# Kernel optimization log

Hardware: AMD Instinct MI355X
Metric: run time of the kernel (lower is better)

Reference implementation:

```python
import jax, jax.numpy as jnp
import numpy as np

B, C, H, W = 32, 512, 32, 32
HEADS = 8
HD = C // HEADS  # 64
BN_EPS = 1e-5


def setup_inputs() -> dict:
    key = jax.random.key(0)
    ks = jax.random.split(key, 8)
    s = 0.02  # trunc_normal std for Linear weights
    x = jax.random.normal(ks[0], (B, C, H, W), jnp.float32)
    Wq = jax.random.normal(ks[1], (C, C), jnp.float32) * s
    Wk = jax.random.normal(ks[2], (C, C), jnp.float32) * s
    Wv = jax.random.normal(ks[3], (C, C), jnp.float32) * s
    # depthwise 3x3 kernel, kaiming fan_out (fan_out = 3*3*1 per group)
    dw_w = jax.random.normal(ks[4], (C, 1, 3, 3), jnp.float32) * np.sqrt(2.0 / 9.0)
    bn_gamma = jnp.ones((C,), jnp.float32)
    bn_beta = jnp.zeros((C,), jnp.float32)
    temperature = jnp.ones((HEADS, 1, 1), jnp.float32)
    Wp = jax.random.normal(ks[5], (C, C), jnp.float32) * s
    bp = jnp.zeros((C,), jnp.float32)
    return {"x": x, "Wq": Wq, "Wk": Wk, "Wv": Wv, "dw_w": dw_w,
            "bn_gamma": bn_gamma, "bn_beta": bn_beta,
            "temperature": temperature, "Wp": Wp, "bp": bp}


def _l2norm(t):
    # torch F.normalize: x / max(||x||, eps)
    n = jnp.sqrt(jnp.sum(t * t, axis=-1, keepdims=True))
    return t / jnp.maximum(n, 1e-12)


def _forward(x, Wq, Wk, Wv, dw_w, bn_gamma, bn_beta, temperature, Wp, bp):
    b, c, h, w = x.shape
    n = h * w
    x_flat = x.transpose(0, 2, 3, 1).reshape(b, n, c)  # [B,N,C]

    q = (x_flat @ Wq.T).reshape(b, n, HEADS, HD).transpose(0, 2, 3, 1)  # [B,h,d,N]
    k = (x_flat @ Wk.T).reshape(b, n, HEADS, HD).transpose(0, 2, 3, 1)
    q = _l2norm(q)
    k = _l2norm(k)

    attn = jnp.einsum('bhdn,bhen->bhde', q, k) * temperature  # [B,h,d,d]
    attn = jax.nn.softmax(attn, axis=-1)

    v_content = x_flat @ Wv.T  # [B,N,C]

    # gated value path: DWConv -> BatchNorm (batch stats, train mode) -> SiLU
    g = jax.lax.conv_general_dilated(
        x, dw_w, window_strides=(1, 1), padding=((1, 1), (1, 1)),
        feature_group_count=c, dimension_numbers=('NCHW', 'OIHW', 'NCHW'))
    mu = jnp.mean(g, axis=(0, 2, 3), keepdims=True)
    var = jnp.var(g, axis=(0, 2, 3), keepdims=True)
    g = (g - mu) * jax.lax.rsqrt(var + BN_EPS)
    g = g * bn_gamma[None, :, None, None] + bn_beta[None, :, None, None]
    g = g * jax.nn.sigmoid(g)  # SiLU
    v_gate = g.transpose(0, 2, 3, 1).reshape(b, n, c)

    v = (v_content * v_gate).reshape(b, n, HEADS, HD).transpose(0, 2, 3, 1)  # [B,h,d,N]
    out = jnp.einsum('bhde,bhen->bhdn', attn, v)  # [B,h,d,N]
    out = out.transpose(0, 3, 1, 2).reshape(b, n, c)  # [B,N,C]
    out = out @ Wp.T + bp
    return out.reshape(b, h, w, c).transpose(0, 3, 1, 2)  # [B,C,H,W]


def reference(x, Wq, Wk, Wv, dw_w, bn_gamma, bn_beta, temperature, Wp, bp):
    return _forward(x, Wq, Wk, Wv, dw_w, bn_gamma, bn_beta, temperature, Wp, bp)
```

## Files before the change

kernel.cpp:

```cpp
#include <hip/hip_runtime.h>
#include <stdint.h>

#define BATCH 32
#define CCH   512
#define NPIX  1024
#define HEADS 8
#define QKV_M 1536

typedef short bf16x8 __attribute__((ext_vector_type(8)));
typedef float f32x4 __attribute__((ext_vector_type(4)));

__device__ inline float bf2f(unsigned short u) {
  union { float f; uint32_t i; } t; t.i = ((uint32_t)u) << 16; return t.f;
}
__device__ inline unsigned short f2bf(float f) {
  union { float f; uint32_t u; } t; t.f = f;
  uint32_t u = t.u;
  return (unsigned short)((u + 0x7FFFu + ((u >> 16) & 1u)) >> 16);
}

__device__ inline void gl_lds16(const unsigned short* g, unsigned short* l) {
  __builtin_amdgcn_global_load_lds(
      (const __attribute__((address_space(1))) uint32_t*)g,
      (__attribute__((address_space(3))) uint32_t*)l, 16, 0, 0);
}

__global__ void convert_w(const float* __restrict__ Wq, const float* __restrict__ Wk,
                          const float* __restrict__ Wv, const float* __restrict__ Wp,
                          unsigned short* __restrict__ wcat,
                          unsigned short* __restrict__ wpb) {
  int i = (blockIdx.x * 256 + threadIdx.x) * 4;
  union { ushort4 u4; unsigned short s[4]; } o;
  f32x4 a;
  a = *(const f32x4*)&Wq[i];
  for (int j = 0; j < 4; j++) o.s[j] = f2bf(a[j]);
  *(ushort4*)&wcat[i] = o.u4;
  a = *(const f32x4*)&Wk[i];
  for (int j = 0; j < 4; j++) o.s[j] = f2bf(a[j]);
  *(ushort4*)&wcat[CCH * CCH + i] = o.u4;
  a = *(const f32x4*)&Wv[i];
  for (int j = 0; j < 4; j++) o.s[j] = f2bf(a[j]);
  *(ushort4*)&wcat[2 * CCH * CCH + i] = o.u4;
  a = *(const f32x4*)&Wp[i];
  for (int j = 0; j < 4; j++) o.s[j] = f2bf(a[j]);
  *(ushort4*)&wpb[i] = o.u4;
}

__global__ void transpose_f2b(const float* __restrict__ in,
                              unsigned short* __restrict__ out, int R, int Cc) {
  __shared__ float tile[32][33];
  int b = blockIdx.z;
  int c0 = blockIdx.x * 32;
  int r0 = blockIdx.y * 32;
  const float* inb = in + (size_t)b * R * Cc;
  unsigned short* outb = out + (size_t)b * R * Cc;
  int tx = threadIdx.x, ty = threadIdx.y;
  for (int i = 0; i < 4; i++) {
    int r = ty + i * 8;
    tile[r][tx] = inb[(size_t)(r0 + r) * Cc + c0 + tx];
  }
  __syncthreads();
  for (int i = 0; i < 4; i++) {
    int r = ty + i * 8;
    outb[(size_t)(c0 + r) * R + r0 + tx] = f2bf(tile[tx][r]);
  }
}

template <bool OUT_F32>
__launch_bounds__(256)
__global__ void gemm_bt(const unsigned short* __restrict__ A,
                        const unsigned short* __restrict__ X,
                        void* __restrict__ Cout,
                        const float* __restrict__ bias,
                        int M, int N, int K) {
  __shared__ __align__(16) unsigned short As[128 * 32];
  __shared__ __align__(16) unsigned short Bs[128 * 32];
  int b  = blockIdx.z;
  int m0 = blockIdx.y * 128;
  int n0 = blockIdx.x * 128;
  const unsigned short* Xb = X + (size_t)b * N * K;
  int tid = threadIdx.x;
  int lane = tid & 63;
  int wave = tid >> 6;
  int wm = wave >> 1, wn = wave & 1;
  int quad = lane >> 4, l16 = lane & 15;

  f32x4 acc[4][4];
  f32x4 zero = {0.f, 0.f, 0.f, 0.f};
  for (int i = 0; i < 4; i++)
    for (int j = 0; j < 4; j++) acc[i][j] = zero;

  int srow = wave * 32 + (lane >> 2);
  int skp  = (lane & 3) * 8;
  const unsigned short* Ag = A  + (size_t)(m0 + srow) * K + skp;
  const unsigned short* Xg = Xb + (size_t)(n0 + srow) * K + skp;
  unsigned short* Al = &As[wave * 1024];
  unsigned short* Bl = &Bs[wave * 1024];

  for (int k0 = 0; k0 < K; k0 += 32) {
    gl_lds16(Ag + k0,            Al);
    gl_lds16(Ag + 16 * K + k0,   Al + 512);
    gl_lds16(Xg + k0,            Bl);
    gl_lds16(Xg + 16 * K + k0,   Bl + 512);
    __syncthreads();
    bf16x8 af[4], bfr[4];
    for (int i = 0; i < 4; i++)
      af[i] = *(const bf16x8*)&As[(wm * 64 + i * 16 + l16) * 32 + quad * 8];
    for (int j = 0; j < 4; j++)
      bfr[j] = *(const bf16x8*)&Bs[(wn * 64 + j * 16 + l16) * 32 + quad * 8];
    for (int i = 0; i < 4; i++)
      for (int j = 0; j < 4; j++)
        acc[i][j] = __builtin_amdgcn_mfma_f32_16x16x32_bf16(af[i], bfr[j], acc[i][j], 0, 0, 0);
    __syncthreads();
  }

  for (int i = 0; i < 4; i++) {
    int gmb = m0 + wm * 64 + i * 16 + quad * 4;
    for (int j = 0; j < 4; j++) {
      int gn = n0 + wn * 64 + j * 16 + l16;
      for (int r = 0; r < 4; r++) {
        int gm = gmb + r;
        float v = acc[i][j][r];
        if (OUT_F32) {
          v += bias[gm];
          ((float*)Cout)[(size_t)b * M * N + (size_t)gm * N + gn] = v;
        } else {
          ((unsigned short*)Cout)[(size_t)b * M * N + (size_t)gm * N + gn] = f2bf(v);
        }
      }
    }
  }
}

__global__ void l2norm_qk(unsigned short* __restrict__ qkv, int nb) {
  int id = blockIdx.x * 4 + (threadIdx.x >> 6);
  int lane = threadIdx.x & 63;
  int total = nb * CCH;
  int isK = id >= total;
  int r = isK ? id - total : id;
  int b = r >> 9, c = r & 511;
  unsigned short* p = qkv + ((size_t)b * QKV_M + (isK ? CCH : 0) + c) * NPIX;
  union { uint4 q4[2]; unsigned short s[16]; } u;
  u.q4[0] = *(const uint4*)&p[lane * 16];
  u.q4[1] = *(const uint4*)&p[lane * 16 + 8];
  float s = 0.f;
  for (int i = 0; i < 16; i++) { float f = bf2f(u.s[i]); s += f * f; }
  for (int off = 32; off > 0; off >>= 1) s += __shfl_down(s, off);
  s = __shfl(s, 0);
  float scale = 1.f / fmaxf(sqrtf(s), 1e-12f);
  for (int i = 0; i < 16; i++) u.s[i] = f2bf(bf2f(u.s[i]) * scale);
  *(uint4*)&p[lane * 16] = u.q4[0];
  *(uint4*)&p[lane * 16 + 8] = u.q4[1];
}

__global__ void dw_stats(const float* __restrict__ x,
                         const float* __restrict__ wgt,
                         float* __restrict__ s1, float* __restrict__ s2) {
  int c = blockIdx.x, b = blockIdx.y;
  __shared__ __align__(16) float plane[NPIX];
  const float* xp = x + ((size_t)b * CCH + c) * NPIX;
  *(f32x4*)&plane[threadIdx.x * 4] = *(const f32x4*)&xp[threadIdx.x * 4];
  __syncthreads();
  float w[9];
  for (int i = 0; i < 9; i++) w[i] = wgt[c * 9 + i];
  float a1 = 0.f, a2 = 0.f;
  for (int pi = 0; pi < 4; pi++) {
    int p = threadIdx.x + pi * 256;
    int h = p >> 5, wc = p & 31;
    float v = 0.f;
    for (int dh = -1; dh <= 1; dh++)
      for (int dw = -1; dw <= 1; dw++) {
        int hh = h + dh, ww = wc + dw;
        if (hh >= 0 && hh < 32 && ww >= 0 && ww < 32)
          v += w[(dh + 1) * 3 + dw + 1] * plane[hh * 32 + ww];
      }
    a1 += v; a2 += v * v;
  }
  for (int off = 32; off > 0; off >>= 1) {
    a1 += __shfl_down(a1, off);
    a2 += __shfl_down(a2, off);
  }
  __shared__ float r1[4], r2[4];
  int wv = threadIdx.x >> 6;
  if ((threadIdx.x & 63) == 0) { r1[wv] = a1; r2[wv] = a2; }
  __syncthreads();
  if (threadIdx.x == 0) {
    atomicAdd(&s1[c], r1[0] + r1[1] + r1[2] + r1[3]);
    atomicAdd(&s2[c], r2[0] + r2[1] + r2[2] + r2[3]);
  }
}

__global__ void gate_apply(const float* __restrict__ x,
                           const float* __restrict__ wgt,
                           const float* __restrict__ s1, const float* __restrict__ s2,
                           const float* __restrict__ gamma,
                           const float* __restrict__ beta,
                           unsigned short* __restrict__ qkv) {
  int c = blockIdx.x, b = blockIdx.y;
  __shared__ __align__(16) float plane[NPIX];
  const float* xp = x + ((size_t)b * CCH + c) * NPIX;
  unsigned short* vp = qkv + ((size_t)b * QKV_M + 2 * CCH + c) * NPIX;
  *(f32x4*)&plane[threadIdx.x * 4] = *(const f32x4*)&xp[threadIdx.x * 4];
  __syncthreads();
  float w[9];
  for (int i = 0; i < 9; i++) w[i] = wgt[c * 9 + i];
  const float invn = 1.f / 32768.f;
  float mean = s1[c] * invn;
  float var = fmaxf(s2[c] * invn - mean * mean, 0.f);
  float rstd = rsqrtf(var + 1e-5f);
  float ga = gamma[c], be = beta[c];
  for (int pi = 0; pi < 4; pi++) {
    int p = threadIdx.x + pi * 256;
    int h = p >> 5, wc = p & 31;
    float val = 0.f;
    for (int dh = -1; dh <= 1; dh++)
      for (int dw = -1; dw <= 1; dw++) {
        int hh = h + dh, ww = wc + dw;
        if (hh >= 0 && hh < 32 && ww >= 0 && ww < 32)
          val += w[(dh + 1) * 3 + dw + 1] * plane[hh * 32 + ww];
      }
    float g = (val - mean) * rstd * ga + be;
    float sg = g / (1.f + __expf(-g));
    vp[p] = f2bf(bf2f(vp[p]) * sg);
  }
}

__launch_bounds__(256)
__global__ void attn_k(const unsigned short* __restrict__ qkv,
                       const float* __restrict__ temp,
                       unsigned short* __restrict__ aoT) {
  int bh = blockIdx.x;
  int b = bh >> 3, h = bh & 7;
  const unsigned short* Q = qkv + ((size_t)b * QKV_M + h * 64) * NPIX;
  const unsigned short* K = Q + (size_t)CCH * NPIX;
  const unsigned short* V = Q + (size_t)2 * CCH * NPIX;
  unsigned short* Ob = aoT + (size_t)b * NPIX * CCH + h * 64;
  int tid = threadIdx.x, lane = tid & 63, wave = tid >> 6;
  int quad = lane >> 4, l16 = lane & 15;

  __shared__ __align__(16) float Sf[64][65];
  __shared__ __align__(16) unsigned short Ps[64][72];
  __shared__ __align__(16) unsigned short Vt[4][16][72];
  __shared__ float redm[4][64], reds[4][64];

  f32x4 zero = {0.f, 0.f, 0.f, 0.f};
  f32x4 acc[4];
  for (int j = 0; j < 4; j++) acc[j] = zero;
  for (int n0 = 0; n0 < NPIX; n0 += 32) {
    bf16x8 a = *(const bf16x8*)&Q[(size_t)(wave * 16 + l16) * NPIX + n0 + quad * 8];
    for (int j = 0; j < 4; j++) {
      bf16x8 bb = *(const bf16x8*)&K[(size_t)(j * 16 + l16) * NPIX + n0 + quad * 8];
      acc[j] = __builtin_amdgcn_mfma_f32_16x16x32_bf16(a, bb, acc[j], 0, 0, 0);
    }
  }
  float tmp = temp[h];
  for (int j = 0; j < 4; j++)
    for (int r = 0; r < 4; r++)
      Sf[wave * 16 + quad * 4 + r][j * 16 + l16] = acc[j][r] * tmp;
  __syncthreads();

  {
    int row = tid & 63, seg = tid >> 6;
    float pm = -1e30f;
    for (int i = 0; i < 16; i++) pm = fmaxf(pm, Sf[row][seg * 16 + i]);
    redm[seg][row] = pm;
    __syncthreads();
    float m = fmaxf(fmaxf(redm[0][row], redm[1][row]),
                    fmaxf(redm[2][row], redm[3][row]));
    float ps = 0.f;
    for (int i = 0; i < 16; i++) ps += __expf(Sf[row][seg * 16 + i] - m);
    reds[seg][row] = ps;
    __syncthreads();
    float inv = 1.f / (reds[0][row] + reds[1][row] + reds[2][row] + reds[3][row]);
    for (int i = 0; i < 16; i++)
      Ps[row][seg * 16 + i] = f2bf(__expf(Sf[row][seg * 16 + i] - m) * inv);
  }
  __syncthreads();

  bf16x8 Pf[4][2];
  for (int j = 0; j < 4; j++)
    for (int ks = 0; ks < 2; ks++)
      Pf[j][ks] = *(const bf16x8*)&Ps[j * 16 + l16][ks * 32 + quad * 8];

  int e1 = lane >> 1, noff = (lane & 1) * 8;
  for (int nt = 0; nt < 16; nt++) {
    int n0 = wave * 256 + nt * 16;
    union { uint4 q; unsigned short s[8]; } g0, g1;
    g0.q = *(const uint4*)&V[(size_t)e1 * NPIX + n0 + noff];
    g1.q = *(const uint4*)&V[(size_t)(e1 + 32) * NPIX + n0 + noff];
    for (int jj = 0; jj < 8; jj++) {
      Vt[wave][noff + jj][e1]      = g0.s[jj];
      Vt[wave][noff + jj][e1 + 32] = g1.s[jj];
    }
    __builtin_amdgcn_sched_barrier(0);
    bf16x8 Af0 = *(const bf16x8*)&Vt[wave][l16][quad * 8];
    bf16x8 Af1 = *(const bf16x8*)&Vt[wave][l16][32 + quad * 8];
    f32x4 oacc[4];
    for (int j = 0; j < 4; j++) {
      oacc[j] = __builtin_amdgcn_mfma_f32_16x16x32_bf16(Af0, Pf[j][0], zero, 0, 0, 0);
      oacc[j] = __builtin_amdgcn_mfma_f32_16x16x32_bf16(Af1, Pf[j][1], oacc[j], 0, 0, 0);
    }
    __builtin_amdgcn_sched_barrier(0);
    for (int j = 0; j < 4; j++)
      for (int r = 0; r < 4; r++)
        Ob[(size_t)(n0 + quad * 4 + r) * CCH + j * 16 + l16] = f2bf(oacc[j][r]);
  }
}

extern "C" void kernel_launch(void* const* d_in, const int* in_sizes, int n_in,
                              void* d_out, int out_size, void* d_ws, size_t ws_size,
                              hipStream_t stream) {
  const float* x     = (const float*)d_in[0];
  const float* Wq    = (const float*)d_in[1];
  const float* Wk    = (const float*)d_in[2];
  const float* Wv    = (const float*)d_in[3];
  const float* dww   = (const float*)d_in[4];
  const float* gamma = (const float*)d_in[5];
  const float* beta  = (const float*)d_in[6];
  const float* temp  = (const float*)d_in[7];
  const float* Wp    = (const float*)d_in[8];
  const float* bp    = (const float*)d_in[9];
  float* out = (float*)d_out;

  char* ws = (char*)d_ws;
  unsigned short* wcat = (unsigned short*)ws;
  unsigned short* wpb  = wcat + (size_t)QKV_M * CCH;
  float* s1 = (float*)(wpb + (size_t)CCH * CCH);
  float* s2 = s1 + CCH;
  char* dyn = (char*)(s2 + CCH);
  size_t fixed = (size_t)(dyn - ws);
  size_t per_b = ((size_t)NPIX * CCH + (size_t)QKV_M * NPIX) * 2;
  int BC = BATCH;
  while (BC > 1 && fixed + (size_t)BC * per_b > ws_size) BC >>= 1;
  unsigned short* xT  = (unsigned short*)dyn;
  unsigned short* qkv = xT + (size_t)BC * NPIX * CCH;

  convert_w<<<CCH * CCH / 1024, 256, 0, stream>>>(Wq, Wk, Wv, Wp, wcat, wpb);
  hipMemsetAsync(s1, 0, 2 * CCH * sizeof(float), stream);
  dw_stats<<<dim3(CCH, BATCH), 256, 0, stream>>>(x, dww, s1, s2);

  for (int b0 = 0; b0 < BATCH; b0 += BC) {
    const float* xc = x + (size_t)b0 * CCH * NPIX;
    float* outc = out + (size_t)b0 * CCH * NPIX;
    transpose_f2b<<<dim3(NPIX / 32, CCH / 32, BC), dim3(32, 8), 0, stream>>>(
        xc, xT, CCH, NPIX);
    gemm_bt<false><<<dim3(NPIX / 128, QKV_M / 128, BC), 256, 0, stream>>>(
        wcat, xT, qkv, nullptr, QKV_M, NPIX, CCH);
    l2norm_qk<<<BC * 256, 256, 0, stream>>>(qkv, BC);
    gate_apply<<<dim3(CCH, BC), 256, 0, stream>>>(xc, dww, s1, s2, gamma, beta, qkv);
    attn_k<<<BC * HEADS, 256, 0, stream>>>(qkv, temp, xT);
    gemm_bt<true><<<dim3(NPIX / 128, CCH / 128, BC), 256, 0, stream>>>(
        wpb, xT, outc, bp, CCH, NPIX, CCH);
  }
}
```

Before: 350.9 us.

## Fold L2 norm into attention scores, split attention, widen GEMM K-tile with swizzle

Drops the separate l2norm pass over Q and K. Row norms are now taken from the diagonal MFMA products inside the score kernel and applied as scales to the 64x64 score matrix. Attention is split into a score/softmax kernel writing P to workspace and a P·V kernel launched with four times as many blocks, which prefetches V and stages output through LDS for coalesced 16-byte stores. The GEMM now loads a 64-wide K tile with an XOR-swizzled LDS layout, halving barrier count and reducing bank conflicts. The norms come from bf16 unnormalized values rather than normalized-then-rounded ones, so numerics shift slightly, and P adds a small workspace round trip.

```diff
diff --git a/kernel.cpp b/kernel.cpp
--- a/kernel.cpp
+++ b/kernel.cpp
@@ -73,8 +73,8 @@
                         void* __restrict__ Cout,
                         const float* __restrict__ bias,
                         int M, int N, int K) {
-  __shared__ __align__(16) unsigned short As[128 * 32];
-  __shared__ __align__(16) unsigned short Bs[128 * 32];
+  __shared__ __align__(16) unsigned short As[128 * 64];
+  __shared__ __align__(16) unsigned short Bs[128 * 64];
   int b  = blockIdx.z;
   int m0 = blockIdx.y * 128;
   int n0 = blockIdx.x * 128;
@@ -90,27 +90,31 @@
   for (int i = 0; i < 4; i++)
     for (int j = 0; j < 4; j++) acc[i][j] = zero;
 
-  int srow = wave * 32 + (lane >> 2);
-  int skp  = (lane & 3) * 8;
-  const unsigned short* Ag = A  + (size_t)(m0 + srow) * K + skp;
-  const unsigned short* Xg = Xb + (size_t)(n0 + srow) * K + skp;
-  unsigned short* Al = &As[wave * 1024];
-  unsigned short* Bl = &Bs[wave * 1024];
-
-  for (int k0 = 0; k0 < K; k0 += 32) {
-    gl_lds16(Ag + k0,            Al);
-    gl_lds16(Ag + 16 * K + k0,   Al + 512);
-    gl_lds16(Xg + k0,            Bl);
-    gl_lds16(Xg + 16 * K + k0,   Bl + 512);
+  int r8 = lane >> 3;
+  int sw = ((lane & 7) ^ r8) * 8;
+  const unsigned short* Ag = A  + (size_t)(m0 + wave * 32 + r8) * K + sw;
+  const unsigned short* Xg = Xb + (size_t)(n0 + wave * 32 + r8) * K + sw;
+  unsigned short* Al = &As[wave * 32 * 64];
+  unsigned short* Bl = &Bs[wave * 32 * 64];
+
+  for (int k0 = 0; k0 < K; k0 += 64) {
+    for (int i = 0; i < 4; i++) {
+      gl_lds16(Ag + k0 + i * 8 * K, Al + i * 8 * 64);
+      gl_lds16(Xg + k0 + i * 8 * K, Bl + i * 8 * 64);
+    }
     __syncthreads();
-    bf16x8 af[4], bfr[4];
-    for (int i = 0; i < 4; i++)
-      af[i] = *(const bf16x8*)&As[(wm * 64 + i * 16 + l16) * 32 + quad * 8];
-    for (int j = 0; j < 4; j++)
-      bfr[j] = *(const bf16x8*)&Bs[(wn * 64 + j * 16 + l16) * 32 + quad * 8];
-    for (int i = 0; i < 4; i++)
-      for (int j = 0; j < 4; j++)
-        acc[i][j] = __builtin_amdgcn_mfma_f32_16x16x32_bf16(af[i], bfr[j], acc[i][j], 0, 0, 0);
+    bf16x8 af[2][4], bfr[2][4];
+    for (int ks = 0; ks < 2; ks++)
+      for (int i = 0; i < 4; i++) {
+        int ch = ((ks * 4 + quad) ^ (l16 & 7)) * 8;
+        af[ks][i]  = *(const bf16x8*)&As[(wm * 64 + i * 16 + l16) * 64 + ch];
+        bfr[ks][i] = *(const bf16x8*)&Bs[(wn * 64 + i * 16 + l16) * 64 + ch];
+      }
+    for (int ks = 0; ks < 2; ks++)
+      for (int i = 0; i < 4; i++)
+        for (int j = 0; j < 4; j++)
+          acc[i][j] = __builtin_amdgcn_mfma_f32_16x16x32_bf16(
+              af[ks][i], bfr[ks][j], acc[i][j], 0, 0, 0);
     __syncthreads();
   }
 
@@ -130,27 +134,6 @@
       }
     }
   }
-}
-
-__global__ void l2norm_qk(unsigned short* __restrict__ qkv, int nb) {
-  int id = blockIdx.x * 4 + (threadIdx.x >> 6);
-  int lane = threadIdx.x & 63;
-  int total = nb * CCH;
-  int isK = id >= total;
-  int r = isK ? id - total : id;
-  int b = r >> 9, c = r & 511;
-  unsigned short* p = qkv + ((size_t)b * QKV_M + (isK ? CCH : 0) + c) * NPIX;
-  union { uint4 q4[2]; unsigned short s[16]; } u;
-  u.q4[0] = *(const uint4*)&p[lane * 16];
-  u.q4[1] = *(const uint4*)&p[lane * 16 + 8];
-  float s = 0.f;
-  for (int i = 0; i < 16; i++) { float f = bf2f(u.s[i]); s += f * f; }
-  for (int off = 32; off > 0; off >>= 1) s += __shfl_down(s, off);
-  s = __shfl(s, 0);
-  float scale = 1.f / fmaxf(sqrtf(s), 1e-12f);
-  for (int i = 0; i < 16; i++) u.s[i] = f2bf(bf2f(u.s[i]) * scale);
-  *(uint4*)&p[lane * 16] = u.q4[0];
-  *(uint4*)&p[lane * 16 + 8] = u.q4[1];
 }
 
 __global__ void dw_stats(const float* __restrict__ x,
@@ -226,73 +209,110 @@
 }
 
 __launch_bounds__(256)
-__global__ void attn_k(const unsigned short* __restrict__ qkv,
+__global__ void attn_s(const unsigned short* __restrict__ qkv,
                        const float* __restrict__ temp,
-                       unsigned short* __restrict__ aoT) {
+                       unsigned short* __restrict__ P) {
   int bh = blockIdx.x;
   int b = bh >> 3, h = bh & 7;
   const unsigned short* Q = qkv + ((size_t)b * QKV_M + h * 64) * NPIX;
   const unsigned short* K = Q + (size_t)CCH * NPIX;
-  const unsigned short* V = Q + (size_t)2 * CCH * NPIX;
+  int tid = threadIdx.x, lane = tid & 63, wave = tid >> 6;
+  int quad = lane >> 4, l16 = lane & 15;
+
+  __shared__ __align__(16) float Sf[64][65];
+  __shared__ float qq[64], kk[64], invq[64], invk[64];
+  __shared__ float redm[4][64], reds[4][64];
+
+  f32x4 zero = {0.f, 0.f, 0.f, 0.f};
+  f32x4 acc[4], accQ = zero, accK = zero;
+  for (int j = 0; j < 4; j++) acc[j] = zero;
+  for (int n0 = 0; n0 < NPIX; n0 += 32) {
+    bf16x8 a  = *(const bf16x8*)&Q[(size_t)(wave * 16 + l16) * NPIX + n0 + quad * 8];
+    bf16x8 ak = *(const bf16x8*)&K[(size_t)(wave * 16 + l16) * NPIX + n0 + quad * 8];
+    accQ = __builtin_amdgcn_mfma_f32_16x16x32_bf16(a, a, accQ, 0, 0, 0);
+    accK = __builtin_amdgcn_mfma_f32_16x16x32_bf16(ak, ak, accK, 0, 0, 0);
+    for (int j = 0; j < 4; j++) {
+      bf16x8 bb = *(const bf16x8*)&K[(size_t)(j * 16 + l16) * NPIX + n0 + quad * 8];
+      acc[j] = __builtin_amdgcn_mfma_f32_16x16x32_bf16(a, bb, acc[j], 0, 0, 0);
+    }
+  }
+  for (int j = 0; j < 4; j++)
+    for (int r = 0; r < 4; r++)
+      Sf[wave * 16 + quad * 4 + r][j * 16 + l16] = acc[j][r];
+  for (int r = 0; r < 4; r++)
+    if (l16 == quad * 4 + r) {
+      qq[wave * 16 + l16] = accQ[r];
+      kk[wave * 16 + l16] = accK[r];
+    }
+  __syncthreads();
+  if (tid < 64) invq[tid] = 1.f / fmaxf(sqrtf(qq[tid]), 1e-12f);
+  else if (tid < 128) invk[tid - 64] = 1.f / fmaxf(sqrtf(kk[tid - 64]), 1e-12f);
+  __syncthreads();
+
+  int row = tid & 63, seg = tid >> 6;
+  float fq = temp[h] * invq[row];
+  float v[16], pm = -1e30f;
+  for (int i = 0; i < 16; i++) {
+    v[i] = Sf[row][seg * 16 + i] * fq * invk[seg * 16 + i];
+    pm = fmaxf(pm, v[i]);
+  }
+  redm[seg][row] = pm;
+  __syncthreads();
+  float m = fmaxf(fmaxf(redm[0][row], redm[1][row]),
+                  fmaxf(redm[2][row], redm[3][row]));
+  float ps = 0.f;
+  for (int i = 0; i < 16; i++) { v[i] = __expf(v[i] - m); ps += v[i]; }
+  reds[seg][row] = ps;
+  __syncthreads();
+  float inv = 1.f / (reds[0][row] + reds[1][row] + reds[2][row] + reds[3][row]);
+  union { uint4 q4[2]; unsigned short s[16]; } u;
+  for (int i = 0; i < 16; i++) u.s[i] = f2bf(v[i] * inv);
+  unsigned short* Pp = P + ((size_t)bh * 64 + row) * 64 + seg * 16;
+  *(uint4*)&Pp[0] = u.q4[0];
+  *(uint4*)&Pp[8] = u.q4[1];
+}
+
+__launch_bounds__(256)
+__global__ void attn_o(const unsigned short* __restrict__ qkv,
+                       const unsigned short* __restrict__ P,
+                       unsigned short* __restrict__ aoT) {
+  int blk = blockIdx.x;
+  int nc = blk & 3, bh = blk >> 2;
+  int b = bh >> 3, h = bh & 7;
+  const unsigned short* V = qkv + ((size_t)b * QKV_M + 2 * CCH + h * 64) * NPIX;
   unsigned short* Ob = aoT + (size_t)b * NPIX * CCH + h * 64;
   int tid = threadIdx.x, lane = tid & 63, wave = tid >> 6;
   int quad = lane >> 4, l16 = lane & 15;
 
-  __shared__ __align__(16) float Sf[64][65];
-  __shared__ __align__(16) unsigned short Ps[64][72];
   __shared__ __align__(16) unsigned short Vt[4][16][72];
-  __shared__ float redm[4][64], reds[4][64];
-
-  f32x4 zero = {0.f, 0.f, 0.f, 0.f};
-  f32x4 acc[4];
-  for (int j = 0; j < 4; j++) acc[j] = zero;
-  for (int n0 = 0; n0 < NPIX; n0 += 32) {
-    bf16x8 a = *(const bf16x8*)&Q[(size_t)(wave * 16 + l16) * NPIX + n0 + quad * 8];
-    for (int j = 0; j < 4; j++) {
-      bf16x8 bb = *(const bf16x8*)&K[(size_t)(j * 16 + l16) * NPIX + n0 + quad * 8];
-      acc[j] = __builtin_amdgcn_mfma_f32_16x16x32_bf16(a, bb, acc[j], 0, 0, 0);
-    }
-  }
-  float tmp = temp[h];
-  for (int j = 0; j < 4; j++)
-    for (int r = 0; r < 4; r++)
-      Sf[wave * 16 + quad * 4 + r][j * 16 + l16] = acc[j][r] * tmp;
-  __syncthreads();
-
-  {
-    int row = tid & 63, seg = tid >> 6;
-    float pm = -1e30f;
-    for (int i = 0; i < 16; i++) pm = fmaxf(pm, Sf[row][seg * 16 + i]);
-    redm[seg][row] = pm;
-    __syncthreads();
-    float m = fmaxf(fmaxf(redm[0][row], redm[1][row]),
-                    fmaxf(redm[2][row], redm[3][row]));
-    float ps = 0.f;
-    for (int i = 0; i < 16; i++) ps += __expf(Sf[row][seg * 16 + i] - m);
-    reds[seg][row] = ps;
-    __syncthreads();
-    float inv = 1.f / (reds[0][row] + reds[1][row] + reds[2][row] + reds[3][row]);
-    for (int i = 0; i < 16; i++)
-      Ps[row][seg * 16 + i] = f2bf(__expf(Sf[row][seg * 16 + i] - m) * inv);
-  }
-  __syncthreads();
-
+  __shared__ __align__(16) unsigned short Ot[4][16][72];
+
+  const unsigned short* Pb = P + (size_t)bh * 64 * 64;
   bf16x8 Pf[4][2];
   for (int j = 0; j < 4; j++)
     for (int ks = 0; ks < 2; ks++)
-      Pf[j][ks] = *(const bf16x8*)&Ps[j * 16 + l16][ks * 32 + quad * 8];
-
+      Pf[j][ks] = *(const bf16x8*)&Pb[(j * 16 + l16) * 64 + ks * 32 + quad * 8];
+
+  f32x4 zero = {0.f, 0.f, 0.f, 0.f};
   int e1 = lane >> 1, noff = (lane & 1) * 8;
-  for (int nt = 0; nt < 16; nt++) {
-    int n0 = wave * 256 + nt * 16;
-    union { uint4 q; unsigned short s[8]; } g0, g1;
-    g0.q = *(const uint4*)&V[(size_t)e1 * NPIX + n0 + noff];
-    g1.q = *(const uint4*)&V[(size_t)(e1 + 32) * NPIX + n0 + noff];
+  int nbase = nc * 256 + wave * 64;
+  int orow = lane >> 3, ocol = (lane & 7) * 8;
+
+  union { uint4 q; unsigned short s[8]; } g0, g1, c0, c1;
+  g0.q = *(const uint4*)&V[(size_t)e1 * NPIX + nbase + noff];
+  g1.q = *(const uint4*)&V[(size_t)(e1 + 32) * NPIX + nbase + noff];
+#pragma unroll
+  for (int nt = 0; nt < 4; nt++) {
+    int n0 = nbase + nt * 16;
+    c0 = g0; c1 = g1;
+    if (nt < 3) {
+      g0.q = *(const uint4*)&V[(size_t)e1 * NPIX + n0 + 16 + noff];
+      g1.q = *(const uint4*)&V[(size_t)(e1 + 32) * NPIX + n0 + 16 + noff];
+    }
     for (int jj = 0; jj < 8; jj++) {
-      Vt[wave][noff + jj][e1]      = g0.s[jj];
-      Vt[wave][noff + jj][e1 + 32] = g1.s[jj];
-    }
-    __builtin_amdgcn_sched_barrier(0);
+      Vt[wave][noff + jj][e1]      = c0.s[jj];
+      Vt[wave][noff + jj][e1 + 32] = c1.s[jj];
+    }
     bf16x8 Af0 = *(const bf16x8*)&Vt[wave][l16][quad * 8];
     bf16x8 Af1 = *(const bf16x8*)&Vt[wave][l16][32 + quad * 8];
     f32x4 oacc[4];
@@ -300,10 +320,13 @@
       oacc[j] = __builtin_amdgcn_mfma_f32_16x16x32_bf16(Af0, Pf[j][0], zero, 0, 0, 0);
       oacc[j] = __builtin_amdgcn_mfma_f32_16x16x32_bf16(Af1, Pf[j][1], oacc[j], 0, 0, 0);
     }
-    __builtin_amdgcn_sched_barrier(0);
     for (int j = 0; j < 4; j++)
       for (int r = 0; r < 4; r++)
-        Ob[(size_t)(n0 + quad * 4 + r) * CCH + j * 16 + l16] = f2bf(oacc[j][r]);
+        Ot[wave][quad * 4 + r][j * 16 + l16] = f2bf(oacc[j][r]);
+    uint4 o0 = *(const uint4*)&Ot[wave][orow][ocol];
+    uint4 o1 = *(const uint4*)&Ot[wave][orow + 8][ocol];
+    *(uint4*)&Ob[(size_t)(n0 + orow) * CCH + ocol] = o0;
+    *(uint4*)&Ob[(size_t)(n0 + orow + 8) * CCH + ocol] = o1;
   }
 }
 
@@ -327,7 +350,8 @@
   unsigned short* wpb  = wcat + (size_t)QKV_M * CCH;
   float* s1 = (float*)(wpb + (size_t)CCH * CCH);
   float* s2 = s1 + CCH;
-  char* dyn = (char*)(s2 + CCH);
+  unsigned short* Pbuf = (unsigned short*)(s2 + CCH);
+  char* dyn = (char*)(Pbuf + (size_t)BATCH * HEADS * 64 * 64);
   size_t fixed = (size_t)(dyn - ws);
   size_t per_b = ((size_t)NPIX * CCH + (size_t)QKV_M * NPIX) * 2;
   int BC = BATCH;
@@ -346,9 +370,9 @@
         xc, xT, CCH, NPIX);
     gemm_bt<false><<<dim3(NPIX / 128, QKV_M / 128, BC), 256, 0, stream>>>(
         wcat, xT, qkv, nullptr, QKV_M, NPIX, CCH);
-    l2norm_qk<<<BC * 256, 256, 0, stream>>>(qkv, BC);
+    attn_s<<<BC * HEADS, 256, 0, stream>>>(qkv, temp, Pbuf);
     gate_apply<<<dim3(CCH, BC), 256, 0, stream>>>(xc, dww, s1, s2, gamma, beta, qkv);
-    attn_k<<<BC * HEADS, 256, 0, stream>>>(qkv, temp, xT);
+    attn_o<<<BC * HEADS * 4, 256, 0, stream>>>(qkv, Pbuf, xT);
     gemm_bt<true><<<dim3(NPIX / 128, CCH / 128, BC), 256, 0, stream>>>(
         wpb, xT, outc, bp, CCH, NPIX, CCH);
   }
```

Measured after the change: 336.2 us. 1.04x faster.
